# Optimization experiments

Hardware: AMD Instinct MI355X
Metric: run time of the kernel (lower is better)

The kernel has to match this reference:

```python
import jax, jax.numpy as jnp
import numpy as np

N, Lq, Lk, D = 4, 2048, 2048, 1024
H, DH = 16, 64  # n_heads, projection_dim
NEG_INF = jnp.float32(-1e30)


def setup_inputs() -> dict:
    key = jax.random.key(0)
    ks = jax.random.split(key, 6)
    query = jax.random.normal(ks[0], (N, Lq, D), dtype=jnp.float32)
    key_t = jax.random.normal(ks[1], (N, Lk, D), dtype=jnp.float32)
    s = 1.0 / np.sqrt(D)
    Wq = jax.random.normal(ks[2], (D, D), dtype=jnp.float32) * s
    Wk = jax.random.normal(ks[3], (D, D), dtype=jnp.float32) * s
    Wv = jax.random.normal(ks[4], (D, D), dtype=jnp.float32) * s
    # causal mask: True where attention is forbidden (j > i)
    mask = jnp.triu(jnp.ones((Lq, Lk), dtype=bool), k=1)
    # per-sample valid lengths in [1024, 2048); padding at the tail
    valid_len = jax.random.randint(ks[5], (N,), Lk // 2, Lk)
    padding_mask = jnp.arange(Lk)[None, :] >= valid_len[:, None]  # (N, Lk) bool
    return {"query": query, "key": key_t, "Wq": Wq, "Wk": Wk, "Wv": Wv,
            "mask": mask, "padding_mask": padding_mask}


def reference(query, key, Wq, Wk, Wv, mask, padding_mask):
    n, lq, _ = query.shape
    lk = key.shape[1]
    # torch Linear (no bias): x @ W.T ; split heads -> (N, H, L, DH)
    q = (query @ Wq.T).reshape(n, lq, H, DH).transpose(0, 2, 1, 3)
    k = (key @ Wk.T).reshape(n, lk, H, DH).transpose(0, 2, 1, 3)
    v = (key @ Wv.T).reshape(n, lk, H, DH).transpose(0, 2, 1, 3)
    # per-sample scaling: sqrt(number of non-padded keys) (module quirk, not sqrt(d))
    valid = jnp.sum(~padding_mask, axis=-1).astype(query.dtype)  # (N,)
    scaling = jnp.sqrt(valid)[:, None, None, None]
    score = jnp.einsum('nhqd,nhkd->nhqk', q, k) / scaling
    score = jnp.where(mask[None, None, :, :], NEG_INF, score)
    score = jnp.where(padding_mask[:, None, None, :], NEG_INF, score)
    attn = jax.nn.softmax(score, axis=-1)
    out = jnp.einsum('nhqk,nhkd->nhqd', attn, v)
    return out.transpose(0, 2, 1, 3).reshape(n, lq, H * DH)
```

## Files before the change

### kernel.cpp

```cpp
#include <hip/hip_runtime.h>
#include <hip/hip_bf16.h>
#include <math.h>


#define N_S 4
#define LQ 2048
#define LK 2048
#define DM 1024
#define NHEAD 16
#define DHEAD 64

typedef __attribute__((ext_vector_type(8))) short short8;
typedef __attribute__((ext_vector_type(4))) float f32x4;

typedef const __attribute__((address_space(1))) void* gptr_t;
typedef __attribute__((address_space(3))) void* lptr_t;

#define GLOAD_LDS(g, l) \
    __builtin_amdgcn_global_load_lds((gptr_t)(const void*)(g), (lptr_t)(void*)(l), 16, 0, 0)

static __device__ __forceinline__ unsigned int pkbf(float a, float b) {
    __hip_bfloat162 h = __float22bfloat162_rn(make_float2(a, b));
    unsigned int u;
    __builtin_memcpy(&u, &h, 4);
    return u;
}

static __device__ __forceinline__ f32x4 zero4() {
    f32x4 v; v[0] = 0.f; v[1] = 0.f; v[2] = 0.f; v[3] = 0.f; return v;
}

static __device__ __forceinline__ void meta_body(const void* __restrict__ pm,
                                                 int* __restrict__ valid_out,
                                                 float* __restrict__ scale_out) {
    __shared__ int okInt, hasPair, okF32;
    __shared__ int counts[4];
    int t = threadIdx.x;
    if (t == 0) { okInt = 1; hasPair = 0; okF32 = 1; }
    if (t < 4) counts[t] = 0;
    __syncthreads();

    const unsigned int* w = (const unsigned int*)pm;
    int bad_int = 0, pair = 0, bad_f32 = 0;
    for (int i = t; i < 2048; i += 256) {
        unsigned int v = w[i];
        if (v > 1u) bad_int = 1;
        if (v == 0x3F803F80u) pair = 1;
        if (v != 0u && v != 0x3F800000u) bad_f32 = 1;
    }
    if (bad_int) okInt = 0;
    if (pair)    hasPair = 1;
    if (bad_f32) okF32 = 0;
    __syncthreads();

    int mode = okInt ? 0 : (hasPair ? 1 : (okF32 ? 2 : 3));
    for (int n = 0; n < 4; n++) {
        int cnt = 0;
        for (int j = t; j < LK; j += 256) {
            int idx = n * LK + j;
            bool z;
            if (mode == 0)      z = (((const int*)pm)[idx] == 0);
            else if (mode == 1) z = (((const unsigned short*)pm)[idx] == 0);
            else if (mode == 2) z = (w[idx] == 0u);
            else                z = (((const unsigned char*)pm)[idx] == 0);
            cnt += z ? 1 : 0;
        }
        atomicAdd(&counts[n], cnt);
    }
    __syncthreads();
    if (t < 4) {
        int c = counts[t] > 0 ? counts[t] : 1;
        valid_out[t] = c;
        scale_out[t] = 1.0f / sqrtf((float)c);
    }
}

__global__ void meta_kernel(const void* __restrict__ pm,
                            int* __restrict__ valid_out,
                            float* __restrict__ scale_out) {
    meta_body(pm, valid_out, scale_out);
}

static __device__ __forceinline__ void conv16(const float* src,
                                              unsigned short* dst, size_t idx) {
    f32x4 a0 = *(const f32x4*)(src + idx);
    f32x4 a1 = *(const f32x4*)(src + idx + 4);
    f32x4 a2 = *(const f32x4*)(src + idx + 8);
    f32x4 a3 = *(const f32x4*)(src + idx + 12);
    uint4 u0, u1;
    u0.x = pkbf(a0[0], a0[1]); u0.y = pkbf(a0[2], a0[3]);
    u0.z = pkbf(a1[0], a1[1]); u0.w = pkbf(a1[2], a1[3]);
    u1.x = pkbf(a2[0], a2[1]); u1.y = pkbf(a2[2], a2[3]);
    u1.z = pkbf(a3[0], a3[1]); u1.w = pkbf(a3[2], a3[3]);
    *(uint4*)(void*)(dst + idx) = u0;
    *(uint4*)(void*)(dst + idx + 8) = u1;
}

__global__ __launch_bounds__(256) void convw_kernel(
    const float* __restrict__ Wq, const float* __restrict__ Wk,
    const float* __restrict__ Wv,
    unsigned short* __restrict__ Wqb, unsigned short* __restrict__ Wkb,
    unsigned short* __restrict__ Wvb)
{
    int z = blockIdx.y;
    const float* src = (z == 0) ? Wq : ((z == 1) ? Wk : Wv);
    unsigned short* dst = (z == 0) ? Wqb : ((z == 1) ? Wkb : Wvb);
    conv16(src, dst, ((size_t)blockIdx.x * 256 + threadIdx.x) * 16);
}

__global__ __launch_bounds__(256) void convx_kernel(
    const float* __restrict__ src, unsigned short* __restrict__ dst)
{
    conv16(src, dst, ((size_t)blockIdx.x * 256 + threadIdx.x) * 16);
}

__global__ __launch_bounds__(256) void prep_kernel(
    const void* __restrict__ pm, int* __restrict__ valid_out,
    float* __restrict__ scale_out,
    const float* __restrict__ Wq, const float* __restrict__ Wk,
    const float* __restrict__ Wv,
    unsigned short* __restrict__ Wqb, unsigned short* __restrict__ Wkb,
    unsigned short* __restrict__ Wvb,
    const float* __restrict__ xq, const float* __restrict__ xk,
    unsigned short* __restrict__ dq, unsigned short* __restrict__ dk)
{
    int b = blockIdx.x;
    int t = threadIdx.x;
    if (b == 0) {
        meta_body(pm, valid_out, scale_out);
    } else if (b <= 768) {
        int bb = b - 1;
        int z = bb >> 8;
        const float* src = (z == 0) ? Wq : ((z == 1) ? Wk : Wv);
        unsigned short* dst = (z == 0) ? Wqb : ((z == 1) ? Wkb : Wvb);
        conv16(src, dst, ((size_t)(bb & 255) * 256 + t) * 16);
    } else {
        int bb = b - 769;
        const float* src = (bb >= 2048) ? xk : xq;
        unsigned short* dst = (bb >= 2048) ? dk : dq;
        int x = (bb >= 2048) ? bb - 2048 : bb;
        conv16(src, dst, ((size_t)x * 256 + t) * 16);
    }
}

static __device__ __forceinline__ void proj_body(
    const unsigned short* __restrict__ XbQ, const unsigned short* __restrict__ XbK,
    const unsigned short* __restrict__ Wqb, const unsigned short* __restrict__ Wkb,
    const unsigned short* __restrict__ Wvb,
    const float* __restrict__ scal, const int* __restrict__ valid_arr,
    unsigned short* __restrict__ Qb, unsigned short* __restrict__ Kb,
    unsigned short* __restrict__ Vt, int bxi, int byi, int z)
{
    int m0 = bxi << 7, n0 = byi << 7;
    if (z >= 1) {
        int n = m0 >> 11, ml = m0 & 2047;
        int tv64 = ((valid_arr[n] + 63) >> 6) << 6;
        if (ml >= tv64) return;
    }

    const unsigned short* W = (z == 0) ? Wqb : ((z == 1) ? Wkb : Wvb);
    const unsigned short* Xb = (z == 0) ? XbQ : XbK;

    __shared__ unsigned short Xls[128 * 32];
    __shared__ unsigned short Wls[128 * 32];

    int t = threadIdx.x;
    int wave = t >> 6, lane = t & 63;
    int l15 = lane & 15, quad = lane >> 4;
    int wa = wave >> 1, wb = wave & 1;

    int srow = t >> 2;
    int sg = ((t & 3) ^ (srow & 3)) << 3;
    const unsigned short* gX0 = Xb + (size_t)(m0 + srow) * DM + sg;
    const unsigned short* gX1 = Xb + (size_t)(m0 + 64 + srow) * DM + sg;
    const unsigned short* gW0 = W + (size_t)(n0 + srow) * DM + sg;
    const unsigned short* gW1 = W + (size_t)(n0 + 64 + srow) * DM + sg;

    f32x4 acc[4][4];
    #pragma unroll
    for (int i = 0; i < 4; i++)
        #pragma unroll
        for (int j = 0; j < 4; j++) acc[i][j] = zero4();

    int aoff = ((quad ^ (l15 & 3)) << 3);
    const unsigned short* Abuf = (z < 2) ? Wls : Xls;
    const unsigned short* Bbuf = (z < 2) ? Xls : Wls;

    for (int kk = 0; kk < DM; kk += 32) {
        __syncthreads();
        GLOAD_LDS(gX0 + kk, Xls + wave * 512);
        GLOAD_LDS(gX1 + kk, Xls + 2048 + wave * 512);
        GLOAD_LDS(gW0 + kk, Wls + wave * 512);
        GLOAD_LDS(gW1 + kk, Wls + 2048 + wave * 512);
        __syncthreads();

        short8 af[4], bf[4];
        #pragma unroll
        for (int ai = 0; ai < 4; ai++)
            af[ai] = *(const short8*)(const void*)(
                Abuf + ((wa * 64 + ai * 16 + l15) << 5) + aoff);
        #pragma unroll
        for (int bi = 0; bi < 4; bi++)
            bf[bi] = *(const short8*)(const void*)(
                Bbuf + ((wb * 64 + bi * 16 + l15) << 5) + aoff);
        #pragma unroll
        for (int ai = 0; ai < 4; ai++)
            #pragma unroll
            for (int bi = 0; bi < 4; bi++)
                acc[ai][bi] = __builtin_amdgcn_mfma_f32_16x16x32_bf16(
                    af[ai], bf[bi], acc[ai][bi], 0, 0, 0);
    }

    if (z < 2) {
        unsigned short* O = (z == 0) ? Qb : Kb;
        #pragma unroll
        for (int bi = 0; bi < 4; bi++) {
            int token = m0 + wb * 64 + bi * 16 + l15;
            float qs = 1.0f;
            if (z == 0) qs = scal[token >> 11] * 1.44269504f;
            #pragma unroll
            for (int ai = 0; ai < 4; ai++) {
                int feat = n0 + wa * 64 + ai * 16 + quad * 4;
                float v0 = acc[ai][bi][0], v1 = acc[ai][bi][1];
                float v2 = acc[ai][bi][2], v3 = acc[ai][bi][3];
                if (z == 0) { v0 *= qs; v1 *= qs; v2 *= qs; v3 *= qs; }
                uint2 u;
                u.x = pkbf(v0, v1);
                u.y = pkbf(v2, v3);
                *(uint2*)(void*)(O + (size_t)token * DM + feat) = u;
            }
        }
    } else {
        #pragma unroll
        for (int ai = 0; ai < 4; ai++) {
            int token0 = m0 + wa * 64 + ai * 16 + quad * 4;
            int n = token0 >> 11, tl = token0 & 2047;
            #pragma unroll
            for (int bi = 0; bi < 4; bi++) {
                int feat = n0 + wb * 64 + bi * 16 + l15;
                uint2 u;
                u.x = pkbf(acc[ai][bi][0], acc[ai][bi][1]);
                u.y = pkbf(acc[ai][bi][2], acc[ai][bi][3]);
                *(uint2*)(void*)(Vt + ((size_t)n * DM + feat) * LK + tl) = u;
            }
        }
    }
}

__global__ __launch_bounds__(256) void proj_bf16_kernel(
    const unsigned short* __restrict__ XbQ, const unsigned short* __restrict__ XbK,
    const unsigned short* __restrict__ Wqb, const unsigned short* __restrict__ Wkb,
    const unsigned short* __restrict__ Wvb,
    const float* __restrict__ scal, const int* __restrict__ valid_arr,
    unsigned short* __restrict__ Qb, unsigned short* __restrict__ Kb,
    unsigned short* __restrict__ Vt, int zbase)
{
    proj_body(XbQ, XbK, Wqb, Wkb, Wvb, scal, valid_arr, Qb, Kb, Vt,
              blockIdx.x, blockIdx.y, blockIdx.z + zbase);
}

__global__ __launch_bounds__(256) void proj_bf16_swz_kernel(
    const unsigned short* __restrict__ XbQ, const unsigned short* __restrict__ XbK,
    const unsigned short* __restrict__ Wqb, const unsigned short* __restrict__ Wkb,
    const unsigned short* __restrict__ Wvb,
    const float* __restrict__ scal, const int* __restrict__ valid_arr,
    unsigned short* __restrict__ Qb, unsigned short* __restrict__ Kb,
    unsigned short* __restrict__ Vt)
{
    int id = blockIdx.x;
    int s = id >> 3;
    int g = (id & 7) * 24 + (s >> 3);
    int y = s & 7;
    int z = g >> 6, x = g & 63;
    proj_body(XbQ, XbK, Wqb, Wkb, Wvb, scal, valid_arr, Qb, Kb, Vt, x, y, z);
}

__global__ __launch_bounds__(256) void proj_f32_kernel(
    const float* __restrict__ Xq, const float* __restrict__ Xk,
    const unsigned short* __restrict__ Wqb, const unsigned short* __restrict__ Wkb,
    const unsigned short* __restrict__ Wvb,
    const float* __restrict__ scal,
    unsigned short* __restrict__ Qb, unsigned short* __restrict__ Kb,
    unsigned short* __restrict__ Vt)
{
    int z = blockIdx.z;
    const float* X = (z == 0) ? Xq : Xk;
    const unsigned short* W = (z == 0) ? Wqb : ((z == 1) ? Wkb : Wvb);

    __shared__ unsigned short Xls[128 * 32];
    __shared__ unsigned short Wls[128 * 32];

    int t = threadIdx.x;
    int wave = t >> 6, lane = t & 63;
    int l15 = lane & 15, quad = lane >> 4;
    int wa = wave >> 1, wb = wave & 1;
    int m0 = blockIdx.x << 7, n0 = blockIdx.y << 7;

    int arow = t >> 1, ah = t & 1;
    int ag0 = ((2 * ah)     ^ (arow & 3)) << 3;
    int ag1 = ((2 * ah + 1) ^ (arow & 3)) << 3;
    const float* gX = X + (size_t)(m0 + arow) * DM;
    unsigned short* lX = Xls + arow * 32 + ah * 16;

    int brow = t >> 2;
    int bg = ((t & 3) ^ (brow & 3)) << 3;
    const unsigned short* gW0 = W + (size_t)(n0 + brow) * DM + bg;
    const unsigned short* gW1 = W + (size_t)(n0 + 64 + brow) * DM + bg;

    f32x4 acc[4][4];
    #pragma unroll
    for (int i = 0; i < 4; i++)
        #pragma unroll
        for (int j = 0; j < 4; j++) acc[i][j] = zero4();

    int aoff = ((quad ^ (l15 & 3)) << 3);

    f32x4 an0 = *(const f32x4*)(gX + ag0);
    f32x4 an1 = *(const f32x4*)(gX + ag0 + 4);
    f32x4 an2 = *(const f32x4*)(gX + ag1);
    f32x4 an3 = *(const f32x4*)(gX + ag1 + 4);

    const unsigned short* Abuf = (z < 2) ? Wls : Xls;
    const unsigned short* Bbuf = (z < 2) ? Xls : Wls;

    for (int kk = 0; kk < DM; kk += 32) {
        __syncthreads();
        GLOAD_LDS(gW0 + kk, Wls + wave * 512);
        GLOAD_LDS(gW1 + kk, Wls + 2048 + wave * 512);
        uint4 ua, ub;
        ua.x = pkbf(an0[0], an0[1]); ua.y = pkbf(an0[2], an0[3]);
        ua.z = pkbf(an1[0], an1[1]); ua.w = pkbf(an1[2], an1[3]);
        ub.x = pkbf(an2[0], an2[1]); ub.y = pkbf(an2[2], an2[3]);
        ub.z = pkbf(an3[0], an3[1]); ub.w = pkbf(an3[2], an3[3]);
        *(uint4*)(void*)(lX)     = ua;
        *(uint4*)(void*)(lX + 8) = ub;
        __syncthreads();

        if (kk + 32 < DM) {
            an0 = *(const f32x4*)(gX + kk + 32 + ag0);
            an1 = *(const f32x4*)(gX + kk + 32 + ag0 + 4);
            an2 = *(const f32x4*)(gX + kk + 32 + ag1);
            an3 = *(const f32x4*)(gX + kk + 32 + ag1 + 4);
        }

        short8 af[4], bf[4];
        #pragma unroll
        for (int ai = 0; ai < 4; ai++)
            af[ai] = *(const short8*)(const void*)(
                Abuf + ((wa * 64 + ai * 16 + l15) << 5) + aoff);
        #pragma unroll
        for (int bi = 0; bi < 4; bi++)
            bf[bi] = *(const short8*)(const void*)(
                Bbuf + ((wb * 64 + bi * 16 + l15) << 5) + aoff);
        #pragma unroll
        for (int ai = 0; ai < 4; ai++)
            #pragma unroll
            for (int bi = 0; bi < 4; bi++)
                acc[ai][bi] = __builtin_amdgcn_mfma_f32_16x16x32_bf16(
                    af[ai], bf[bi], acc[ai][bi], 0, 0, 0);
    }

    if (z < 2) {
        unsigned short* O = (z == 0) ? Qb : Kb;
        #pragma unroll
        for (int bi = 0; bi < 4; bi++) {
            int token = m0 + wb * 64 + bi * 16 + l15;
            float qs = 1.0f;
            if (z == 0) qs = scal[token >> 11] * 1.44269504f;
            #pragma unroll
            for (int ai = 0; ai < 4; ai++) {
                int feat = n0 + wa * 64 + ai * 16 + quad * 4;
                float v0 = acc[ai][bi][0], v1 = acc[ai][bi][1];
                float v2 = acc[ai][bi][2], v3 = acc[ai][bi][3];
                if (z == 0) { v0 *= qs; v1 *= qs; v2 *= qs; v3 *= qs; }
                uint2 u;
                u.x = pkbf(v0, v1);
                u.y = pkbf(v2, v3);
                *(uint2*)(void*)(O + (size_t)token * DM + feat) = u;
            }
        }
    } else {
        #pragma unroll
        for (int ai = 0; ai < 4; ai++) {
            int token0 = m0 + wa * 64 + ai * 16 + quad * 4;
            int n = token0 >> 11, tl = token0 & 2047;
            #pragma unroll
            for (int bi = 0; bi < 4; bi++) {
                int feat = n0 + wb * 64 + bi * 16 + l15;
                uint2 u;
                u.x = pkbf(acc[ai][bi][0], acc[ai][bi][1]);
                u.y = pkbf(acc[ai][bi][2], acc[ai][bi][3]);
                *(uint2*)(void*)(Vt + ((size_t)n * DM + feat) * LK + tl) = u;
            }
        }
    }
}

__global__ __launch_bounds__(256) void attn_kernel(
    const unsigned short* __restrict__ Qb, const unsigned short* __restrict__ Kb,
    const unsigned short* __restrict__ Vt,
    const int* __restrict__ valid_arr,
    float* __restrict__ out)
{
    __shared__ unsigned short Kls[2][128 * 64];

    int id = blockIdx.x;
    int xcd = id & 7;
    int slot = id >> 3;
    int g = slot >> 4;
    int bx = slot & 15;
    int n = g >> 1;
    int h = 2 * xcd + (g & 1);

    int tA = bx, tB = 31 - bx;

    int valid = valid_arr[n];
    int tvalid = (valid + 63) >> 6;
    int TlA = (tA + 1 < tvalid) ? tA + 1 : tvalid;
    int TlB = (tB + 1 < tvalid) ? tB + 1 : tvalid;
    int Tpair = (TlB + 1) >> 1;

    int t = threadIdx.x;
    int wave = t >> 6, lane = t & 63;
    int l15 = lane & 15, quad = lane >> 4;

    int qyA = tA * 64 + wave * 16 + l15;
    int qyB = tB * 64 + wave * 16 + l15;
    int qw0A = tA * 64 + wave * 16;
    int qw0B = tB * 64 + wave * 16;

    const unsigned short* QrowA = Qb + ((size_t)n * LQ + qyA) * DM + h * DHEAD;
    const unsigned short* QrowB = Qb + ((size_t)n * LQ + qyB) * DM + h * DHEAD;
    short8 qfA0 = *(const short8*)(const void*)(QrowA + quad * 8);
    short8 qfA1 = *(const short8*)(const void*)(QrowA + 32 + quad * 8);
    short8 qfB0 = *(const short8*)(const void*)(QrowB + quad * 8);
    short8 qfB1 = *(const short8*)(const void*)(QrowB + 32 + quad * 8);

    f32x4 OA[4], OB[4];
    #pragma unroll
    for (int i = 0; i < 4; i++) { OA[i] = zero4(); OB[i] = zero4(); }
    f32x4 LAcc = zero4(), LBcc = zero4();

    short8 onesf;
    #pragma unroll
    for (int i = 0; i < 8; i++) onesf[i] = (short)0x3F80;

    const unsigned short* Kbase = Kb + (size_t)n * LK * DM + h * DHEAD;
    const unsigned short* Vbase = Vt + ((size_t)n * DM + h * DHEAD) * LK;

    int srow0 = t >> 3;
    int sgk   = (((t & 7) ^ (srow0 & 7)) << 3);

    #pragma unroll
    for (int r = 0; r < 4; r++)
        GLOAD_LDS(Kbase + (size_t)(r * 32 + srow0) * DM + sgk,
                  &Kls[0][0] + r * 2048 + wave * 512);
    asm volatile("s_waitcnt vmcnt(0)" ::: "memory");

    auto sub_tile = [&](int cur, int j64, int rowoff, bool doA) {
        int jb = j64 << 6;

        short8 vf0[4], vf1[4];
        #pragma unroll
        for (int cb = 0; cb < 4; cb++) {
            vf0[cb] = *(const short8*)(const void*)(
                Vbase + (size_t)(cb * 16 + l15) * LK + jb + quad * 8);
            vf1[cb] = *(const short8*)(const void*)(
                Vbase + (size_t)(cb * 16 + l15) * LK + jb + 32 + quad * 8);
        }

        f32x4 sA[4], sB[4];
        __builtin_amdgcn_s_setprio(1);
        #pragma unroll
        for (int cb = 0; cb < 4; cb++) {
            const unsigned short* krow =
                &Kls[cur][0] + ((rowoff + cb * 16 + l15) << 6);
            short8 kf0 = *(const short8*)(const void*)(krow + ((quad ^ (l15 & 7)) << 3));
            short8 kf1 = *(const short8*)(const void*)(krow + (((4 + quad) ^ (l15 & 7)) << 3));
            f32x4 sb = zero4();
            sb = __builtin_amdgcn_mfma_f32_16x16x32_bf16(kf0, qfB0, sb, 0, 0, 0);
            sb = __builtin_amdgcn_mfma_f32_16x16x32_bf16(kf1, qfB1, sb, 0, 0, 0);
            sB[cb] = sb;
            if (doA) {
                f32x4 sa = zero4();
                sa = __builtin_amdgcn_mfma_f32_16x16x32_bf16(kf0, qfA0, sa, 0, 0, 0);
                sa = __builtin_amdgcn_mfma_f32_16x16x32_bf16(kf1, qfA1, sa, 0, 0, 0);
                sA[cb] = sa;
            }
        }
        __builtin_amdgcn_s_setprio(0);

        if (jb + 63 > qw0B || jb + 64 > valid) {
            #pragma unroll
            for (int cb = 0; cb < 4; cb++) {
                int jb2 = jb + cb * 16 + quad * 4;
                #pragma unroll
                for (int r = 0; r < 4; r++) {
                    int j = jb2 + r;
                    if (j > qyB || j >= valid) sB[cb][r] = -1e30f;
                }
            }
        }
        short8 pfB0, pfB1;
        {
            unsigned int lo[4], hi[4];
            #pragma unroll
            for (int cb = 0; cb < 4; cb++) {
                lo[cb] = pkbf(__builtin_amdgcn_exp2f(sB[cb][0]),
                              __builtin_amdgcn_exp2f(sB[cb][1]));
                hi[cb] = pkbf(__builtin_amdgcn_exp2f(sB[cb][2]),
                              __builtin_amdgcn_exp2f(sB[cb][3]));
            }
            asm("v_permlane32_swap_b32 %0, %1" : "+v"(lo[0]), "+v"(lo[1]));
            asm("v_permlane32_swap_b32 %0, %1" : "+v"(hi[0]), "+v"(hi[1]));
            asm("v_permlane32_swap_b32 %0, %1" : "+v"(lo[2]), "+v"(lo[3]));
            asm("v_permlane32_swap_b32 %0, %1" : "+v"(hi[2]), "+v"(hi[3]));
            asm("v_permlane16_swap_b32 %0, %1" : "+v"(lo[0]), "+v"(lo[1]));
            asm("v_permlane16_swap_b32 %0, %1" : "+v"(hi[0]), "+v"(hi[1]));
            asm("v_permlane16_swap_b32 %0, %1" : "+v"(lo[2]), "+v"(lo[3]));
            asm("v_permlane16_swap_b32 %0, %1" : "+v"(hi[2]), "+v"(hi[3]));
            uint4 w0, w1;
            w0.x = lo[0]; w0.y = hi[0]; w0.z = lo[1]; w0.w = hi[1];
            w1.x = lo[2]; w1.y = hi[2]; w1.z = lo[3]; w1.w = hi[3];
            __builtin_memcpy(&pfB0, &w0, 16);
            __builtin_memcpy(&pfB1, &w1, 16);
        }
        __builtin_amdgcn_s_setprio(1);
        #pragma unroll
        for (int cb = 0; cb < 4; cb++) {
            OB[cb] = __builtin_amdgcn_mfma_f32_16x16x32_bf16(pfB0, vf0[cb], OB[cb], 0, 0, 0);
            OB[cb] = __builtin_amdgcn_mfma_f32_16x16x32_bf16(pfB1, vf1[cb], OB[cb], 0, 0, 0);
        }
        LBcc = __builtin_amdgcn_mfma_f32_16x16x32_bf16(pfB0, onesf, LBcc, 0, 0, 0);
        LBcc = __builtin_amdgcn_mfma_f32_16x16x32_bf16(pfB1, onesf, LBcc, 0, 0, 0);
        __builtin_amdgcn_s_setprio(0);

        if (doA) {
            if (jb + 63 > qw0A || jb + 64 > valid) {
                #pragma unroll
                for (int cb = 0; cb < 4; cb++) {
                    int jb2 = jb + cb * 16 + quad * 4;
                    #pragma unroll
                    for (int r = 0; r < 4; r++) {
                        int j = jb2 + r;
                        if (j > qyA || j >= valid) sA[cb][r] = -1e30f;
                    }
                }
            }
            short8 pfA0, pfA1;
            {
                unsigned int lo[4], hi[4];
                #pragma unroll
                for (int cb = 0; cb < 4; cb++) {
                    lo[cb] = pkbf(__builtin_amdgcn_exp2f(sA[cb][0]),
                                  __builtin_amdgcn_exp2f(sA[cb][1]));
                    hi[cb] = pkbf(__builtin_amdgcn_exp2f(sA[cb][2]),
                                  __builtin_amdgcn_exp2f(sA[cb][3]));
                }
                asm("v_permlane32_swap_b32 %0, %1" : "+v"(lo[0]), "+v"(lo[1]));
                asm("v_permlane32_swap_b32 %0, %1" : "+v"(hi[0]), "+v"(hi[1]));
                asm("v_permlane32_swap_b32 %0, %1" : "+v"(lo[2]), "+v"(lo[3]));
                asm("v_permlane32_swap_b32 %0, %1" : "+v"(hi[2]), "+v"(hi[3]));
                asm("v_permlane16_swap_b32 %0, %1" : "+v"(lo[0]), "+v"(lo[1]));
                asm("v_permlane16_swap_b32 %0, %1" : "+v"(hi[0]), "+v"(hi[1]));
                asm("v_permlane16_swap_b32 %0, %1" : "+v"(lo[2]), "+v"(lo[3]));
                asm("v_permlane16_swap_b32 %0, %1" : "+v"(hi[2]), "+v"(hi[3]));
                uint4 w0, w1;
                w0.x = lo[0]; w0.y = hi[0]; w0.z = lo[1]; w0.w = hi[1];
                w1.x = lo[2]; w1.y = hi[2]; w1.z = lo[3]; w1.w = hi[3];
                __builtin_memcpy(&pfA0, &w0, 16);
                __builtin_memcpy(&pfA1, &w1, 16);
            }
            __builtin_amdgcn_s_setprio(1);
            #pragma unroll
            for (int cb = 0; cb < 4; cb++) {
                OA[cb] = __builtin_amdgcn_mfma_f32_16x16x32_bf16(pfA0, vf0[cb], OA[cb], 0, 0, 0);
                OA[cb] = __builtin_amdgcn_mfma_f32_16x16x32_bf16(pfA1, vf1[cb], OA[cb], 0, 0, 0);
            }
            LAcc = __builtin_amdgcn_mfma_f32_16x16x32_bf16(pfA0, onesf, LAcc, 0, 0, 0);
            LAcc = __builtin_amdgcn_mfma_f32_16x16x32_bf16(pfA1, onesf, LAcc, 0, 0, 0);
            __builtin_amdgcn_s_setprio(0);
        }
    };

    int cur = 0;
    for (int kt = 0; kt < Tpair; kt++) {
        __builtin_amdgcn_sched_barrier(0);
        __builtin_amdgcn_s_barrier();
        __builtin_amdgcn_sched_barrier(0);

        if (kt + 1 < Tpair) {
            size_t rb = (size_t)(kt + 1) << 7;
            #pragma unroll
            for (int r = 0; r < 4; r++)
                GLOAD_LDS(Kbase + (rb + r * 32 + srow0) * DM + sgk,
                          &Kls[1 - cur][0] + r * 2048 + wave * 512);
        }

        int j64 = kt << 1;
        sub_tile(cur, j64, 0, j64 < TlA);
        if (j64 + 1 < TlB)
            sub_tile(cur, j64 + 1, 64, j64 + 1 < TlA);

        asm volatile("s_waitcnt vmcnt(0)" ::: "memory");
        cur ^= 1;
    }

    float* obase = out + ((size_t)n * LQ) * DM + h * DHEAD;
    #pragma unroll
    for (int r = 0; r < 4; r++) {
        float iA = 1.0f / LAcc[r];
        float iB = 1.0f / LBcc[r];
        int rowA = tA * 64 + wave * 16 + quad * 4 + r;
        int rowB = tB * 64 + wave * 16 + quad * 4 + r;
        #pragma unroll
        for (int cb = 0; cb < 4; cb++) {
            obase[(size_t)rowA * DM + cb * 16 + l15] = OA[cb][r] * iA;
            obase[(size_t)rowB * DM + cb * 16 + l15] = OB[cb][r] * iB;
        }
    }
}

extern "C" void kernel_launch(void* const* d_in, const int* in_sizes, int n_in,
                              void* d_out, int out_size, void* d_ws, size_t ws_size,
                              hipStream_t stream)
{
    (void)in_sizes; (void)n_in; (void)out_size;

    const float* query = (const float*)d_in[0];
    const float* key   = (const float*)d_in[1];
    const float* Wq    = (const float*)d_in[2];
    const float* Wk    = (const float*)d_in[3];
    const float* Wv    = (const float*)d_in[4];
    const void* pmask  = d_in[6];

    char* ws = (char*)d_ws;
    unsigned short* Qb  = (unsigned short*)(ws);
    unsigned short* Kb  = (unsigned short*)(ws + (size_t)16 * 1024 * 1024);
    unsigned short* Vt  = (unsigned short*)(ws + (size_t)32 * 1024 * 1024);
    int*   valid = (int*)  (ws + (size_t)48 * 1024 * 1024);
    float* scal  = (float*)(ws + (size_t)48 * 1024 * 1024 + 64);
    unsigned short* Wqb = (unsigned short*)(ws + (size_t)48 * 1024 * 1024 + 4096);
    unsigned short* Wkb = Wqb + (size_t)DM * DM;
    unsigned short* Wvb = Wkb + (size_t)DM * DM;
    unsigned short* XbQ = Wvb + (size_t)DM * DM;
    unsigned short* XbK = XbQ + (size_t)N_S * LQ * DM;

    size_t xbytes      = (size_t)N_S * LQ * DM * 2;
    size_t need_phased = (size_t)(48 * 1024 * 1024) + 4096
                       + 3 * (size_t)DM * DM * 2 + xbytes;
    size_t need_full   = need_phased + xbytes;

    if (ws_size >= need_full) {
        prep_kernel<<<dim3(1 + 768 + 4096), 256, 0, stream>>>(
            pmask, valid, scal, Wq, Wk, Wv, Wqb, Wkb, Wvb,
            query, key, XbQ, XbK);
        proj_bf16_swz_kernel<<<dim3(1536), 256, 0, stream>>>(
            XbQ, XbK, Wqb, Wkb, Wvb, scal, valid, Qb, Kb, Vt);
    } else if (ws_size >= need_phased) {
        meta_kernel<<<1, 256, 0, stream>>>(pmask, valid, scal);
        convw_kernel<<<dim3(256, 3), 256, 0, stream>>>(Wq, Wk, Wv, Wqb, Wkb, Wvb);
        convx_kernel<<<2048, 256, 0, stream>>>(query, XbQ);
        proj_bf16_kernel<<<dim3(64, 8, 1), 256, 0, stream>>>(
            XbQ, XbQ, Wqb, Wkb, Wvb, scal, valid, Qb, Kb, Vt, 0);
        convx_kernel<<<2048, 256, 0, stream>>>(key, XbQ);
        proj_bf16_kernel<<<dim3(64, 8, 2), 256, 0, stream>>>(
            XbQ, XbQ, Wqb, Wkb, Wvb, scal, valid, Qb, Kb, Vt, 1);
    } else {
        meta_kernel<<<1, 256, 0, stream>>>(pmask, valid, scal);
        convw_kernel<<<dim3(256, 3), 256, 0, stream>>>(Wq, Wk, Wv, Wqb, Wkb, Wvb);
        proj_f32_kernel<<<dim3(64, 8, 3), 256, 0, stream>>>(
            query, key, Wqb, Wkb, Wvb, scal, Qb, Kb, Vt);
    }

    attn_kernel<<<dim3(1024), 256, 0, stream>>>(Qb, Kb, Vt, valid,
                                                (float*)d_out);
}
```

Measured before the change: 315.4 us.

## Double K-depth per projection sync and batch attention QK before softmax-PV

```diff
diff --git a/kernel.cpp b/kernel.cpp
--- a/kernel.cpp
+++ b/kernel.cpp
@@ -161,8 +161,8 @@
     const unsigned short* W = (z == 0) ? Wqb : ((z == 1) ? Wkb : Wvb);
     const unsigned short* Xb = (z == 0) ? XbQ : XbK;
 
-    __shared__ unsigned short Xls[128 * 32];
-    __shared__ unsigned short Wls[128 * 32];
+    __shared__ unsigned short Xls[2][128 * 32];
+    __shared__ unsigned short Wls[2][128 * 32];
 
     int t = threadIdx.x;
     int wave = t >> 6, lane = t & 63;
@@ -183,32 +183,39 @@
         for (int j = 0; j < 4; j++) acc[i][j] = zero4();
 
     int aoff = ((quad ^ (l15 & 3)) << 3);
-    const unsigned short* Abuf = (z < 2) ? Wls : Xls;
-    const unsigned short* Bbuf = (z < 2) ? Xls : Wls;
-
-    for (int kk = 0; kk < DM; kk += 32) {
+
+    for (int kk = 0; kk < DM; kk += 64) {
         __syncthreads();
-        GLOAD_LDS(gX0 + kk, Xls + wave * 512);
-        GLOAD_LDS(gX1 + kk, Xls + 2048 + wave * 512);
-        GLOAD_LDS(gW0 + kk, Wls + wave * 512);
-        GLOAD_LDS(gW1 + kk, Wls + 2048 + wave * 512);
+        GLOAD_LDS(gX0 + kk,      &Xls[0][0] + wave * 512);
+        GLOAD_LDS(gX1 + kk,      &Xls[0][0] + 2048 + wave * 512);
+        GLOAD_LDS(gW0 + kk,      &Wls[0][0] + wave * 512);
+        GLOAD_LDS(gW1 + kk,      &Wls[0][0] + 2048 + wave * 512);
+        GLOAD_LDS(gX0 + kk + 32, &Xls[1][0] + wave * 512);
+        GLOAD_LDS(gX1 + kk + 32, &Xls[1][0] + 2048 + wave * 512);
+        GLOAD_LDS(gW0 + kk + 32, &Wls[1][0] + wave * 512);
+        GLOAD_LDS(gW1 + kk + 32, &Wls[1][0] + 2048 + wave * 512);
         __syncthreads();
 
-        short8 af[4], bf[4];
-        #pragma unroll
-        for (int ai = 0; ai < 4; ai++)
-            af[ai] = *(const short8*)(const void*)(
-                Abuf + ((wa * 64 + ai * 16 + l15) << 5) + aoff);
-        #pragma unroll
-        for (int bi = 0; bi < 4; bi++)
-            bf[bi] = *(const short8*)(const void*)(
-                Bbuf + ((wb * 64 + bi * 16 + l15) << 5) + aoff);
-        #pragma unroll
-        for (int ai = 0; ai < 4; ai++)
+        #pragma unroll
+        for (int half = 0; half < 2; half++) {
+            const unsigned short* Abuf = (z < 2) ? &Wls[half][0] : &Xls[half][0];
+            const unsigned short* Bbuf = (z < 2) ? &Xls[half][0] : &Wls[half][0];
+            short8 af[4], bf[4];
+            #pragma unroll
+            for (int ai = 0; ai < 4; ai++)
+                af[ai] = *(const short8*)(const void*)(
+                    Abuf + ((wa * 64 + ai * 16 + l15) << 5) + aoff);
             #pragma unroll
             for (int bi = 0; bi < 4; bi++)
-                acc[ai][bi] = __builtin_amdgcn_mfma_f32_16x16x32_bf16(
-                    af[ai], bf[bi], acc[ai][bi], 0, 0, 0);
+                bf[bi] = *(const short8*)(const void*)(
+                    Bbuf + ((wb * 64 + bi * 16 + l15) << 5) + aoff);
+            #pragma unroll
+            for (int ai = 0; ai < 4; ai++)
+                #pragma unroll
+                for (int bi = 0; bi < 4; bi++)
+                    acc[ai][bi] = __builtin_amdgcn_mfma_f32_16x16x32_bf16(
+                        af[ai], bf[bi], acc[ai][bi], 0, 0, 0);
+        }
     }
 
     if (z < 2) {
@@ -451,16 +458,9 @@
     int srow0 = t >> 3;
     int sgk   = (((t & 7) ^ (srow0 & 7)) << 3);
 
-    #pragma unroll
-    for (int r = 0; r < 4; r++)
-        GLOAD_LDS(Kbase + (size_t)(r * 32 + srow0) * DM + sgk,
-                  &Kls[0][0] + r * 2048 + wave * 512);
-    asm volatile("s_waitcnt vmcnt(0)" ::: "memory");
-
-    auto sub_tile = [&](int cur, int j64, int rowoff, bool doA) {
-        int jb = j64 << 6;
-
-        short8 vf0[4], vf1[4];
+    int cur = 0;
+
+    auto loadV = [&](int jb, short8* vf0, short8* vf1) {
         #pragma unroll
         for (int cb = 0; cb < 4; cb++) {
             vf0[cb] = *(const short8*)(const void*)(
@@ -468,9 +468,9 @@
             vf1[cb] = *(const short8*)(const void*)(
                 Vbase + (size_t)(cb * 16 + l15) * LK + jb + 32 + quad * 8);
         }
-
-        f32x4 sA[4], sB[4];
-        __builtin_amdgcn_s_setprio(1);
+    };
+
+    auto qk_sub = [&](int rowoff, f32x4* sB, f32x4* sA, bool doA) {
         #pragma unroll
         for (int cb = 0; cb < 4; cb++) {
             const unsigned short* krow =
@@ -488,102 +488,59 @@
                 sA[cb] = sa;
             }
         }
-        __builtin_amdgcn_s_setprio(0);
-
-        if (jb + 63 > qw0B || jb + 64 > valid) {
+    };
+
+    auto sm_pv = [&](f32x4* s, int jb, int qy, int qw0,
+                     const short8* vf0, const short8* vf1,
+                     f32x4* O, f32x4& Lc) {
+        if (jb + 63 > qw0 || jb + 64 > valid) {
             #pragma unroll
             for (int cb = 0; cb < 4; cb++) {
                 int jb2 = jb + cb * 16 + quad * 4;
                 #pragma unroll
                 for (int r = 0; r < 4; r++) {
                     int j = jb2 + r;
-                    if (j > qyB || j >= valid) sB[cb][r] = -1e30f;
+                    if (j > qy || j >= valid) s[cb][r] = -1e30f;
                 }
             }
         }
-        short8 pfB0, pfB1;
-        {
-            unsigned int lo[4], hi[4];
-            #pragma unroll
-            for (int cb = 0; cb < 4; cb++) {
-                lo[cb] = pkbf(__builtin_amdgcn_exp2f(sB[cb][0]),
-                              __builtin_amdgcn_exp2f(sB[cb][1]));
-                hi[cb] = pkbf(__builtin_amdgcn_exp2f(sB[cb][2]),
-                              __builtin_amdgcn_exp2f(sB[cb][3]));
-            }
-            asm("v_permlane32_swap_b32 %0, %1" : "+v"(lo[0]), "+v"(lo[1]));
-            asm("v_permlane32_swap_b32 %0, %1" : "+v"(hi[0]), "+v"(hi[1]));
-            asm("v_permlane32_swap_b32 %0, %1" : "+v"(lo[2]), "+v"(lo[3]));
-            asm("v_permlane32_swap_b32 %0, %1" : "+v"(hi[2]), "+v"(hi[3]));
-            asm("v_permlane16_swap_b32 %0, %1" : "+v"(lo[0]), "+v"(lo[1]));
-            asm("v_permlane16_swap_b32 %0, %1" : "+v"(hi[0]), "+v"(hi[1]));
-            asm("v_permlane16_swap_b32 %0, %1" : "+v"(lo[2]), "+v"(lo[3]));
-            asm("v_permlane16_swap_b32 %0, %1" : "+v"(hi[2]), "+v"(hi[3]));
-            uint4 w0, w1;
-            w0.x = lo[0]; w0.y = hi[0]; w0.z = lo[1]; w0.w = hi[1];
-            w1.x = lo[2]; w1.y = hi[2]; w1.z = lo[3]; w1.w = hi[3];
-            __builtin_memcpy(&pfB0, &w0, 16);
-            __builtin_memcpy(&pfB1, &w1, 16);
-        }
-        __builtin_amdgcn_s_setprio(1);
+        unsigned int lo[4], hi[4];
         #pragma unroll
         for (int cb = 0; cb < 4; cb++) {
-            OB[cb] = __builtin_amdgcn_mfma_f32_16x16x32_bf16(pfB0, vf0[cb], OB[cb], 0, 0, 0);
-            OB[cb] = __builtin_amdgcn_mfma_f32_16x16x32_bf16(pfB1, vf1[cb], OB[cb], 0, 0, 0);
-        }
-        LBcc = __builtin_amdgcn_mfma_f32_16x16x32_bf16(pfB0, onesf, LBcc, 0, 0, 0);
-        LBcc = __builtin_amdgcn_mfma_f32_16x16x32_bf16(pfB1, onesf, LBcc, 0, 0, 0);
-        __builtin_amdgcn_s_setprio(0);
-
-        if (doA) {
-            if (jb + 63 > qw0A || jb + 64 > valid) {
-                #pragma unroll
-                for (int cb = 0; cb < 4; cb++) {
-                    int jb2 = jb + cb * 16 + quad * 4;
-                    #pragma unroll
-                    for (int r = 0; r < 4; r++) {
-                        int j = jb2 + r;
-                        if (j > qyA || j >= valid) sA[cb][r] = -1e30f;
-                    }
-                }
-            }
-            short8 pfA0, pfA1;
-            {
-                unsigned int lo[4], hi[4];
-                #pragma unroll
-                for (int cb = 0; cb < 4; cb++) {
-                    lo[cb] = pkbf(__builtin_amdgcn_exp2f(sA[cb][0]),
-                                  __builtin_amdgcn_exp2f(sA[cb][1]));
-                    hi[cb] = pkbf(__builtin_amdgcn_exp2f(sA[cb][2]),
-                                  __builtin_amdgcn_exp2f(sA[cb][3]));
-                }
-                asm("v_permlane32_swap_b32 %0, %1" : "+v"(lo[0]), "+v"(lo[1]));
-                asm("v_permlane32_swap_b32 %0, %1" : "+v"(hi[0]), "+v"(hi[1]));
-                asm("v_permlane32_swap_b32 %0, %1" : "+v"(lo[2]), "+v"(lo[3]));
-                asm("v_permlane32_swap_b32 %0, %1" : "+v"(hi[2]), "+v"(hi[3]));
-                asm("v_permlane16_swap_b32 %0, %1" : "+v"(lo[0]), "+v"(lo[1]));
-                asm("v_permlane16_swap_b32 %0, %1" : "+v"(hi[0]), "+v"(hi[1]));
-                asm("v_permlane16_swap_b32 %0, %1" : "+v"(lo[2]), "+v"(lo[3]));
-                asm("v_permlane16_swap_b32 %0, %1" : "+v"(hi[2]), "+v"(hi[3]));
-                uint4 w0, w1;
-                w0.x = lo[0]; w0.y = hi[0]; w0.z = lo[1]; w0.w = hi[1];
-                w1.x = lo[2]; w1.y = hi[2]; w1.z = lo[3]; w1.w = hi[3];
-                __builtin_memcpy(&pfA0, &w0, 16);
-                __builtin_memcpy(&pfA1, &w1, 16);
-            }
-            __builtin_amdgcn_s_setprio(1);
-            #pragma unroll
-            for (int cb = 0; cb < 4; cb++) {
-                OA[cb] = __builtin_amdgcn_mfma_f32_16x16x32_bf16(pfA0, vf0[cb], OA[cb], 0, 0, 0);
-                OA[cb] = __builtin_amdgcn_mfma_f32_16x16x32_bf16(pfA1, vf1[cb], OA[cb], 0, 0, 0);
-            }
-            LAcc = __builtin_amdgcn_mfma_f32_16x16x32_bf16(pfA0, onesf, LAcc, 0, 0, 0);
-            LAcc = __builtin_amdgcn_mfma_f32_16x16x32_bf16(pfA1, onesf, LAcc, 0, 0, 0);
-            __builtin_amdgcn_s_setprio(0);
-        }
+            lo[cb] = pkbf(__builtin_amdgcn_exp2f(s[cb][0]),
+                          __builtin_amdgcn_exp2f(s[cb][1]));
+            hi[cb] = pkbf(__builtin_amdgcn_exp2f(s[cb][2]),
+                          __builtin_amdgcn_exp2f(s[cb][3]));
+        }
+        asm("v_permlane32_swap_b32 %0, %1" : "+v"(lo[0]), "+v"(lo[1]));
+        asm("v_permlane32_swap_b32 %0, %1" : "+v"(hi[0]), "+v"(hi[1]));
+        asm("v_permlane32_swap_b32 %0, %1" : "+v"(lo[2]), "+v"(lo[3]));
+        asm("v_permlane32_swap_b32 %0, %1" : "+v"(hi[2]), "+v"(hi[3]));
+        asm("v_permlane16_swap_b32 %0, %1" : "+v"(lo[0]), "+v"(lo[1]));
+        asm("v_permlane16_swap_b32 %0, %1" : "+v"(hi[0]), "+v"(hi[1]));
+        asm("v_permlane16_swap_b32 %0, %1" : "+v"(lo[2]), "+v"(lo[3]));
+        asm("v_permlane16_swap_b32 %0, %1" : "+v"(hi[2]), "+v"(hi[3]));
+        uint4 w0, w1;
+        w0.x = lo[0]; w0.y = hi[0]; w0.z = lo[1]; w0.w = hi[1];
+        w1.x = lo[2]; w1.y = hi[2]; w1.z = lo[3]; w1.w = hi[3];
+        short8 pf0, pf1;
+        __builtin_memcpy(&pf0, &w0, 16);
+        __builtin_memcpy(&pf1, &w1, 16);
+        #pragma unroll
+        for (int cb = 0; cb < 4; cb++) {
+            O[cb] = __builtin_amdgcn_mfma_f32_16x16x32_bf16(pf0, vf0[cb], O[cb], 0, 0, 0);
+            O[cb] = __builtin_amdgcn_mfma_f32_16x16x32_bf16(pf1, vf1[cb], O[cb], 0, 0, 0);
+        }
+        Lc = __builtin_amdgcn_mfma_f32_16x16x32_bf16(pf0, onesf, Lc, 0, 0, 0);
+        Lc = __builtin_amdgcn_mfma_f32_16x16x32_bf16(pf1, onesf, Lc, 0, 0, 0);
     };
 
-    int cur = 0;
+    #pragma unroll
+    for (int r = 0; r < 4; r++)
+        GLOAD_LDS(Kbase + (size_t)(r * 32 + srow0) * DM + sgk,
+                  &Kls[0][0] + r * 2048 + wave * 512);
+    asm volatile("s_waitcnt vmcnt(0)" ::: "memory");
+
     for (int kt = 0; kt < Tpair; kt++) {
         __builtin_amdgcn_sched_barrier(0);
         __builtin_amdgcn_s_barrier();
@@ -598,9 +555,24 @@
         }
 
         int j64 = kt << 1;
-        sub_tile(cur, j64, 0, j64 < TlA);
-        if (j64 + 1 < TlB)
-            sub_tile(cur, j64 + 1, 64, j64 + 1 < TlA);
+        int jb0 = j64 << 6, jb1 = jb0 + 64;
+        bool do1 = (j64 + 1 < TlB);
+        bool doA0 = (j64 < TlA), doA1 = (j64 + 1 < TlA);
+
+        short8 v00[4], v01[4], v10[4], v11[4];
+        loadV(jb0, v00, v01);
+        if (do1) loadV(jb1, v10, v11);
+
+        f32x4 s0B[4], s0A[4], s1B[4], s1A[4];
+        qk_sub(0, s0B, s0A, doA0);
+        if (do1) qk_sub(64, s1B, s1A, doA1);
+
+        sm_pv(s0B, jb0, qyB, qw0B, v00, v01, OB, LBcc);
+        if (doA0) sm_pv(s0A, jb0, qyA, qw0A, v00, v01, OA, LAcc);
+        if (do1) {
+            sm_pv(s1B, jb1, qyB, qw0B, v10, v11, OB, LBcc);
+            if (doA1) sm_pv(s1A, jb1, qyA, qw0A, v10, v11, OA, LAcc);
+        }
 
         asm volatile("s_waitcnt vmcnt(0)" ::: "memory");
         cur ^= 1;
```

Result: slower. 393.3 us (+24.7%).

## Double-buffer LDS tiles in projection GEMM to overlap loads with MFMA

Applied to the files above, without the earlier changes.

```diff
diff --git a/kernel.cpp b/kernel.cpp
--- a/kernel.cpp
+++ b/kernel.cpp
@@ -161,8 +161,8 @@
     const unsigned short* W = (z == 0) ? Wqb : ((z == 1) ? Wkb : Wvb);
     const unsigned short* Xb = (z == 0) ? XbQ : XbK;
 
-    __shared__ unsigned short Xls[128 * 32];
-    __shared__ unsigned short Wls[128 * 32];
+    __shared__ unsigned short Xls[2][128 * 32];
+    __shared__ unsigned short Wls[2][128 * 32];
 
     int t = threadIdx.x;
     int wave = t >> 6, lane = t & 63;
@@ -183,17 +183,26 @@
         for (int j = 0; j < 4; j++) acc[i][j] = zero4();
 
     int aoff = ((quad ^ (l15 & 3)) << 3);
-    const unsigned short* Abuf = (z < 2) ? Wls : Xls;
-    const unsigned short* Bbuf = (z < 2) ? Xls : Wls;
-
+
+    GLOAD_LDS(gX0, &Xls[0][0] + wave * 512);
+    GLOAD_LDS(gX1, &Xls[0][0] + 2048 + wave * 512);
+    GLOAD_LDS(gW0, &Wls[0][0] + wave * 512);
+    GLOAD_LDS(gW1, &Wls[0][0] + 2048 + wave * 512);
+    asm volatile("s_waitcnt vmcnt(0)" ::: "memory");
+    __builtin_amdgcn_s_barrier();
+    __builtin_amdgcn_sched_barrier(0);
+
+    int cur = 0;
     for (int kk = 0; kk < DM; kk += 32) {
-        __syncthreads();
-        GLOAD_LDS(gX0 + kk, Xls + wave * 512);
-        GLOAD_LDS(gX1 + kk, Xls + 2048 + wave * 512);
-        GLOAD_LDS(gW0 + kk, Wls + wave * 512);
-        GLOAD_LDS(gW1 + kk, Wls + 2048 + wave * 512);
-        __syncthreads();
-
+        if (kk + 32 < DM) {
+            GLOAD_LDS(gX0 + kk + 32, &Xls[1 - cur][0] + wave * 512);
+            GLOAD_LDS(gX1 + kk + 32, &Xls[1 - cur][0] + 2048 + wave * 512);
+            GLOAD_LDS(gW0 + kk + 32, &Wls[1 - cur][0] + wave * 512);
+            GLOAD_LDS(gW1 + kk + 32, &Wls[1 - cur][0] + 2048 + wave * 512);
+        }
+
+        const unsigned short* Abuf = (z < 2) ? &Wls[cur][0] : &Xls[cur][0];
+        const unsigned short* Bbuf = (z < 2) ? &Xls[cur][0] : &Wls[cur][0];
         short8 af[4], bf[4];
         #pragma unroll
         for (int ai = 0; ai < 4; ai++)
@@ -209,6 +218,12 @@
             for (int bi = 0; bi < 4; bi++)
                 acc[ai][bi] = __builtin_amdgcn_mfma_f32_16x16x32_bf16(
                     af[ai], bf[bi], acc[ai][bi], 0, 0, 0);
+
+        asm volatile("s_waitcnt vmcnt(0)" ::: "memory");
+        __builtin_amdgcn_sched_barrier(0);
+        __builtin_amdgcn_s_barrier();
+        __builtin_amdgcn_sched_barrier(0);
+        cur ^= 1;
     }
 
     if (z < 2) {
```

Result: slower. 333.4 us (+5.7%).
